# Performance work log

Measured on AMD Instinct MI355X. Metric: run time of the kernel, lower is better.

Reference implementation:

```python
import jax, jax.numpy as jnp
import numpy as np

ALPHA = 0.2  # LeakyReLU negative slope

N, Hd, Wd, T, V = 4, 16, 16, 24, 32


def setup_inputs() -> dict:
    key = jax.random.key(0)
    k1, k2, k3 = jax.random.split(key, 3)
    h = jax.random.normal(k1, (N, Hd, Wd, T, V), dtype=jnp.float32)
    W_param = jax.random.normal(k2, (T, T), dtype=jnp.float32) * 0.1
    a_param = jax.random.normal(k3, (2 * Hd * Wd, 1), dtype=jnp.float32) * 0.1
    B_param = jnp.zeros((V, V), dtype=jnp.float32)
    return {"h": h, "W_param": W_param, "a_param": a_param, "B_param": B_param}


def reference(h, W_param, a_param, B_param):
    n, H, W, T_, V_ = h.shape
    hv = jnp.transpose(h, (0, 4, 1, 2, 3))  # (N,V,H,W,T)
    Wh = hv @ W_param                        # (N,V,H,W,T), contracts last dim T

    # batch_prepare_attentional_mechanism_input (faithful to the torch view):
    rep_chunks = jnp.repeat(Wh, V_, axis=1)          # (N,V*V,H,W,T) -> i index
    rep_alt = jnp.tile(Wh, (1, V_, 1, 1, 1))          # (N,V*V,H,W,T) -> j index
    a_input = jnp.concatenate([rep_chunks, rep_alt], axis=-2)  # (N,V*V,H,2W,T)
    a_input = a_input.reshape(n, V_, V_, T_, 2 * H * W)        # raw row-major view

    e = jnp.squeeze(a_input @ a_param, -1)            # (N,V,V,T)
    e = jnp.where(e > 0, e, ALPHA * e)                # LeakyReLU
    att = jax.nn.softmax(e, axis=-1)                  # softmax over T (dim=-1)

    # adjacency: B + I, min-max normalized, symmetric D^{-1/2} A D^{-1/2}
    adj = B_param + 1e-6 + jnp.eye(V_, dtype=h.dtype)
    adj = (adj - adj.min()) / (adj.max() - adj.min())
    dinv = 1.0 / jnp.sqrt(jnp.sum(adj, axis=1))
    adj_norm = adj * dinv[:, None] * dinv[None, :]

    # nested per-node loop collapsed: matmul with diag_embed(att) == per-t scaling
    Whf = Wh.reshape(n, V_, H * W, T_)
    hp = jnp.einsum('njpt,nijt->nipt', Whf, att)      # (N,V,HW,T)
    h2 = jnp.einsum('nipt,iv->nptv', hp, adj_norm)    # (N,HW,T,V)
    h2 = h2.reshape(n, H, W, T_, V_)
    return jax.nn.sigmoid(jax.nn.elu(h2))
```

## Files before the change

kernel.cpp:

```cpp
#include <hip/hip_runtime.h>
#include <math.h>

#define ALPHA 0.2f

#define NB 4
#define TT 24
#define VV 32
#define HW 256

#define WS_WH    0
#define WS_EPART 786432
#define WS_ATT   983040
#define WS_ADJN  1081344

__global__ __launch_bounds__(256) void k1_wh_e(
    const float* __restrict__ h, const float* __restrict__ Wp,
    const float* __restrict__ ap, float* __restrict__ ws)
{
  __shared__ float WL[576];
  __shared__ float aL[512];
  __shared__ float EiL[768];
  __shared__ float EjL[768];

  const int b   = blockIdx.x;
  const int n   = b >> 5;
  const int pt  = b & 31;
  const int p0  = pt * 8;
  const int tid = threadIdx.x;
  const int v   = tid & 31;
  const int g   = tid >> 5;
  const int p   = p0 + g;

  for (int idx = tid; idx < 576; idx += 256) WL[idx] = Wp[idx];
  for (int idx = tid; idx < 512; idx += 256) aL[idx] = ap[idx];
  for (int idx = tid; idx < 768; idx += 256) { EiL[idx] = 0.f; EjL[idx] = 0.f; }

  float hrow[24];
  const float* hp = h + (size_t)(n * HW + p) * TT * VV + v;
  #pragma unroll
  for (int t2 = 0; t2 < 24; ++t2) hrow[t2] = hp[t2 * 32];

  __syncthreads();

  float acc[24];
  #pragma unroll
  for (int t = 0; t < 24; ++t) acc[t] = 0.f;
  #pragma unroll
  for (int t2 = 0; t2 < 24; ++t2) {
    const float hv = hrow[t2];
    const float4* wrow = (const float4*)&WL[t2 * 24];
    #pragma unroll
    for (int q = 0; q < 6; ++q) {
      float4 w4 = wrow[q];
      acc[q*4+0] += hv * w4.x; acc[q*4+1] += hv * w4.y;
      acc[q*4+2] += hv * w4.z; acc[q*4+3] += hv * w4.w;
    }
  }

  const int hh = p >> 4, w = p & 15;
  const int qi0 = hh * 768 + w * 24;
  const int qj0 = qi0 + 384;
  const int tti0 = qi0 >> 9;
  const int ttj0 = qj0 >> 9;
  const bool cri = (((qi0 + 23) >> 9) != tti0);
  const bool crj = (((qj0 + 23) >> 9) != ttj0);

  float ai0 = 0.f, ai1 = 0.f, aj0 = 0.f, aj1 = 0.f;

  float* whout = ws + WS_WH + (size_t)n * TT * HW * VV + (size_t)p * VV + v;
  #pragma unroll
  for (int t = 0; t < 24; ++t) {
    const float wh = acc[t];
    whout[(size_t)t * HW * VV] = wh;
    const int qi = qi0 + t;
    const float ci = aL[qi & 511] * wh;
    const bool si = ((qi >> 9) != tti0);
    ai0 += si ? 0.f : ci;  ai1 += si ? ci : 0.f;
    const int qj = qj0 + t;
    const float cj = aL[qj & 511] * wh;
    const bool sj = ((qj >> 9) != ttj0);
    aj0 += sj ? 0.f : cj;  aj1 += sj ? cj : 0.f;
  }

  atomicAdd(&EiL[v * 24 + tti0], ai0);
  if (cri) atomicAdd(&EiL[v * 24 + tti0 + 1], ai1);
  atomicAdd(&EjL[v * 24 + ttj0], aj0);
  if (crj) atomicAdd(&EjL[v * 24 + ttj0 + 1], aj1);
  __syncthreads();

  float* ep = ws + WS_EPART + (size_t)b * 1536;
  for (int idx = tid; idx < 768; idx += 256) {
    ep[idx]       = EiL[idx];
    ep[768 + idx] = EjL[idx];
  }
}

__global__ __launch_bounds__(256) void k2_att(
    const float* __restrict__ Bp, float* __restrict__ ws)
{
  __shared__ float E[2 * 32 * 25];
  __shared__ float adjw[1024];
  __shared__ float dinvL[32];
  __shared__ float redmn[4], redmx[4];
  __shared__ float smn, smx;

  const int n = blockIdx.x;
  const int tid = threadIdx.x;

  const float* ep = ws + WS_EPART + (size_t)n * 32 * 1536;
  for (int o = tid; o < 1536; o += 256) {
    float s = 0.f;
    #pragma unroll 4
    for (int k = 0; k < 32; ++k) s += ep[(size_t)k * 1536 + o];
    const int side = o >> 9 >= 1 ? (o >= 768 ? 1 : 0) : 0;
    const int rem = o - (o >= 768 ? 768 : 0);
    const int vv = rem / 24, t = rem - vv * 24;
    E[(o >= 768 ? 800 : 0) + vv * 25 + t] = s;
    (void)side;
  }

  float lmn = 1e30f, lmx = -1e30f;
  if (n == 0) {
    for (int o = tid; o < 1024; o += 256) {
      const int i = o >> 5, j = o & 31;
      const float x = Bp[o] + 1e-6f + (i == j ? 1.f : 0.f);
      adjw[o] = x;
      lmn = fminf(lmn, x); lmx = fmaxf(lmx, x);
    }
    #pragma unroll
    for (int off = 32; off > 0; off >>= 1) {
      lmn = fminf(lmn, __shfl_down(lmn, off));
      lmx = fmaxf(lmx, __shfl_down(lmx, off));
    }
    if ((tid & 63) == 0) { redmn[tid >> 6] = lmn; redmx[tid >> 6] = lmx; }
  }
  __syncthreads();
  if (n == 0 && tid == 0) {
    smn = fminf(fminf(redmn[0], redmn[1]), fminf(redmn[2], redmn[3]));
    smx = fmaxf(fmaxf(redmx[0], redmx[1]), fmaxf(redmx[2], redmx[3]));
  }
  __syncthreads();
  if (n == 0) {
    const float rs = 1.f / (smx - smn);
    for (int o = tid; o < 1024; o += 256) adjw[o] = (adjw[o] - smn) * rs;
  }
  __syncthreads();
  if (n == 0 && tid < 32) {
    float s = 0.f;
    #pragma unroll
    for (int j = 0; j < 32; ++j) s += adjw[tid * 32 + j];
    dinvL[tid] = rsqrtf(s);
  }
  __syncthreads();
  if (n == 0) {
    for (int o = tid; o < 1024; o += 256) {
      const int i = o >> 5, j = o & 31;
      ws[WS_ADJN + o] = adjw[o] * dinvL[i] * dinvL[j];
    }
  }

  for (int pair = tid; pair < 1024; pair += 256) {
    const int i = pair >> 5, j = pair & 31;
    const float* Ei = &E[i * 25];
    const float* Ej = &E[800 + j * 25];
    float ev[24];
    float mx = -1e30f;
    #pragma unroll
    for (int t = 0; t < 24; ++t) {
      float x = Ei[t] + Ej[t];
      x = x > 0.f ? x : ALPHA * x;
      ev[t] = x; mx = fmaxf(mx, x);
    }
    float s = 0.f;
    #pragma unroll
    for (int t = 0; t < 24; ++t) { const float e = __expf(ev[t] - mx); ev[t] = e; s += e; }
    const float r = 1.f / s;
    float* attout = ws + WS_ATT + (size_t)n * TT * 1024 + pair;
    #pragma unroll
    for (int t = 0; t < 24; ++t) attout[(size_t)t * 1024] = ev[t] * r;
  }
}

__global__ __launch_bounds__(256) void k3_out(
    float* __restrict__ out, const float* __restrict__ ws)
{
  __shared__ float attL[1024];
  __shared__ float adjnL[1024];
  __shared__ float MT[1024];
  __shared__ float WhL[8192];

  const int b = blockIdx.x;
  const int n = b / 24, t = b - n * 24;
  const int tid = threadIdx.x;

  const float* attg = ws + WS_ATT + (size_t)(n * 24 + t) * 1024;
  for (int o = tid; o < 1024; o += 256) {
    attL[o]  = attg[o];
    adjnL[o] = ws[WS_ADJN + o];
  }
  const float4* wh4 = (const float4*)(ws + WS_WH + (size_t)(n * 24 + t) * 8192);
  float4* whl4 = (float4*)WhL;
  for (int o = tid; o < 2048; o += 256) whl4[o] = wh4[o];
  __syncthreads();

  for (int o = tid; o < 1024; o += 256) {
    const int j = o >> 5, v = o & 31;
    float s = 0.f;
    #pragma unroll
    for (int i = 0; i < 32; ++i) s += adjnL[i * 32 + v] * attL[i * 32 + j];
    MT[o] = s;
  }
  __syncthreads();

  const int v = tid & 31, g = tid >> 5;
  float mv[32];
  #pragma unroll
  for (int jj = 0; jj < 32; ++jj) mv[jj] = MT[jj * 32 + v];

  float* outg = out + (size_t)n * HW * TT * VV + (size_t)t * VV + v;
  #pragma unroll 4
  for (int k = 0; k < 32; ++k) {
    const int p = (g << 5) + k;
    const float4* wr = (const float4*)&WhL[p * 32];
    float accv = 0.f;
    #pragma unroll
    for (int q = 0; q < 8; ++q) {
      float4 w4 = wr[q];
      accv += w4.x * mv[q*4+0] + w4.y * mv[q*4+1] + w4.z * mv[q*4+2] + w4.w * mv[q*4+3];
    }
    const float e  = accv > 0.f ? accv : (__expf(accv) - 1.f);
    const float sg = 1.f / (1.f + __expf(-e));
    outg[(size_t)p * TT * VV] = sg;
  }
}

extern "C" void kernel_launch(void* const* d_in, const int* in_sizes, int n_in,
                              void* d_out, int out_size, void* d_ws, size_t ws_size,
                              hipStream_t stream) {
  const float* h  = (const float*)d_in[0];
  const float* Wp = (const float*)d_in[1];
  const float* ap = (const float*)d_in[2];
  const float* Bp = (const float*)d_in[3];
  float* out = (float*)d_out;
  float* ws  = (float*)d_ws;

  hipLaunchKernelGGL(k1_wh_e, dim3(NB * 32), dim3(256), 0, stream, h, Wp, ap, ws);
  hipLaunchKernelGGL(k2_att,  dim3(NB),      dim3(256), 0, stream, Bp, ws);
  hipLaunchKernelGGL(k3_out,  dim3(NB * 24), dim3(256), 0, stream, out, ws);
}
```

Before: 104.2 us.

## Fuse attention softmax and adjacency normalization into the output kernel

Merges the per-batch attention kernel and the output kernel into one kernel launched per (batch, t) block. Each block recomputes the E reduction, the adjacency normalization and the softmax for its single t in shared memory, so the attention and adjacency workspace round-trips and one launch go away. In exchange the E partial-sum reduction and the softmax over all 1024 pairs are repeated 24 times per batch, and the previous stage ran on only 4 blocks.

```diff
diff --git a/kernel.cpp b/kernel.cpp
--- a/kernel.cpp
+++ b/kernel.cpp
@@ -10,8 +10,6 @@
 
 #define WS_WH    0
 #define WS_EPART 786432
-#define WS_ATT   983040
-#define WS_ADJN  1081344
 
 __global__ __launch_bounds__(256) void k1_wh_e(
     const float* __restrict__ h, const float* __restrict__ Wp,
@@ -95,70 +93,75 @@
   }
 }
 
-__global__ __launch_bounds__(256) void k2_att(
-    const float* __restrict__ Bp, float* __restrict__ ws)
+__global__ __launch_bounds__(256) void k2_fused(
+    const float* __restrict__ Bp, float* __restrict__ out,
+    const float* __restrict__ ws)
 {
-  __shared__ float E[2 * 32 * 25];
+  __shared__ float E[1600];
   __shared__ float adjw[1024];
+  __shared__ float attL[1024];
+  __shared__ float MT[1024];
+  __shared__ float WhL[8192];
   __shared__ float dinvL[32];
   __shared__ float redmn[4], redmx[4];
   __shared__ float smn, smx;
 
-  const int n = blockIdx.x;
+  const int b = blockIdx.x;
+  const int n = b / 24, t = b - n * 24;
   const int tid = threadIdx.x;
+
+  const float4* wh4 = (const float4*)(ws + WS_WH + (size_t)(n * 24 + t) * 8192);
+  float4* whl4 = (float4*)WhL;
+  for (int o = tid; o < 2048; o += 256) whl4[o] = wh4[o];
 
   const float* ep = ws + WS_EPART + (size_t)n * 32 * 1536;
   for (int o = tid; o < 1536; o += 256) {
     float s = 0.f;
-    #pragma unroll 4
+    #pragma unroll 8
     for (int k = 0; k < 32; ++k) s += ep[(size_t)k * 1536 + o];
-    const int side = o >> 9 >= 1 ? (o >= 768 ? 1 : 0) : 0;
-    const int rem = o - (o >= 768 ? 768 : 0);
-    const int vv = rem / 24, t = rem - vv * 24;
-    E[(o >= 768 ? 800 : 0) + vv * 25 + t] = s;
-    (void)side;
+    const int side = (o >= 768) ? 1 : 0;
+    const int rem = o - side * 768;
+    const int vv = rem / 24, tt = rem - vv * 24;
+    E[side * 800 + vv * 25 + tt] = s;
   }
 
   float lmn = 1e30f, lmx = -1e30f;
-  if (n == 0) {
-    for (int o = tid; o < 1024; o += 256) {
-      const int i = o >> 5, j = o & 31;
-      const float x = Bp[o] + 1e-6f + (i == j ? 1.f : 0.f);
-      adjw[o] = x;
-      lmn = fminf(lmn, x); lmx = fmaxf(lmx, x);
-    }
-    #pragma unroll
-    for (int off = 32; off > 0; off >>= 1) {
-      lmn = fminf(lmn, __shfl_down(lmn, off));
-      lmx = fmaxf(lmx, __shfl_down(lmx, off));
-    }
-    if ((tid & 63) == 0) { redmn[tid >> 6] = lmn; redmx[tid >> 6] = lmx; }
-  }
-  __syncthreads();
-  if (n == 0 && tid == 0) {
+  for (int o = tid; o < 1024; o += 256) {
+    const int i = o >> 5, j = o & 31;
+    const float x = Bp[o] + 1e-6f + (i == j ? 1.f : 0.f);
+    adjw[o] = x;
+    lmn = fminf(lmn, x); lmx = fmaxf(lmx, x);
+  }
+  #pragma unroll
+  for (int off = 32; off > 0; off >>= 1) {
+    lmn = fminf(lmn, __shfl_down(lmn, off));
+    lmx = fmaxf(lmx, __shfl_down(lmx, off));
+  }
+  if ((tid & 63) == 0) { redmn[tid >> 6] = lmn; redmx[tid >> 6] = lmx; }
+  __syncthreads();
+
+  if (tid == 0) {
     smn = fminf(fminf(redmn[0], redmn[1]), fminf(redmn[2], redmn[3]));
     smx = fmaxf(fmaxf(redmx[0], redmx[1]), fmaxf(redmx[2], redmx[3]));
   }
   __syncthreads();
-  if (n == 0) {
-    const float rs = 1.f / (smx - smn);
-    for (int o = tid; o < 1024; o += 256) adjw[o] = (adjw[o] - smn) * rs;
-  }
-  __syncthreads();
-  if (n == 0 && tid < 32) {
+
+  const float rs = 1.f / (smx - smn);
+  for (int o = tid; o < 1024; o += 256) adjw[o] = (adjw[o] - smn) * rs;
+  __syncthreads();
+
+  if (tid < 32) {
     float s = 0.f;
     #pragma unroll
     for (int j = 0; j < 32; ++j) s += adjw[tid * 32 + j];
     dinvL[tid] = rsqrtf(s);
   }
   __syncthreads();
-  if (n == 0) {
-    for (int o = tid; o < 1024; o += 256) {
-      const int i = o >> 5, j = o & 31;
-      ws[WS_ADJN + o] = adjw[o] * dinvL[i] * dinvL[j];
-    }
-  }
-
+
+  for (int o = tid; o < 1024; o += 256) {
+    const int i = o >> 5, j = o & 31;
+    adjw[o] = adjw[o] * dinvL[i] * dinvL[j];
+  }
   for (int pair = tid; pair < 1024; pair += 256) {
     const int i = pair >> 5, j = pair & 31;
     const float* Ei = &E[i * 25];
@@ -166,48 +169,23 @@
     float ev[24];
     float mx = -1e30f;
     #pragma unroll
-    for (int t = 0; t < 24; ++t) {
-      float x = Ei[t] + Ej[t];
+    for (int t2 = 0; t2 < 24; ++t2) {
+      float x = Ei[t2] + Ej[t2];
       x = x > 0.f ? x : ALPHA * x;
-      ev[t] = x; mx = fmaxf(mx, x);
+      ev[t2] = x; mx = fmaxf(mx, x);
     }
     float s = 0.f;
     #pragma unroll
-    for (int t = 0; t < 24; ++t) { const float e = __expf(ev[t] - mx); ev[t] = e; s += e; }
-    const float r = 1.f / s;
-    float* attout = ws + WS_ATT + (size_t)n * TT * 1024 + pair;
-    #pragma unroll
-    for (int t = 0; t < 24; ++t) attout[(size_t)t * 1024] = ev[t] * r;
-  }
-}
-
-__global__ __launch_bounds__(256) void k3_out(
-    float* __restrict__ out, const float* __restrict__ ws)
-{
-  __shared__ float attL[1024];
-  __shared__ float adjnL[1024];
-  __shared__ float MT[1024];
-  __shared__ float WhL[8192];
-
-  const int b = blockIdx.x;
-  const int n = b / 24, t = b - n * 24;
-  const int tid = threadIdx.x;
-
-  const float* attg = ws + WS_ATT + (size_t)(n * 24 + t) * 1024;
-  for (int o = tid; o < 1024; o += 256) {
-    attL[o]  = attg[o];
-    adjnL[o] = ws[WS_ADJN + o];
-  }
-  const float4* wh4 = (const float4*)(ws + WS_WH + (size_t)(n * 24 + t) * 8192);
-  float4* whl4 = (float4*)WhL;
-  for (int o = tid; o < 2048; o += 256) whl4[o] = wh4[o];
+    for (int t2 = 0; t2 < 24; ++t2) { const float e = __expf(ev[t2] - mx); ev[t2] = e; s += e; }
+    attL[pair] = ev[t] / s;
+  }
   __syncthreads();
 
   for (int o = tid; o < 1024; o += 256) {
     const int j = o >> 5, v = o & 31;
     float s = 0.f;
     #pragma unroll
-    for (int i = 0; i < 32; ++i) s += adjnL[i * 32 + v] * attL[i * 32 + j];
+    for (int i = 0; i < 32; ++i) s += adjw[i * 32 + v] * attL[i * 32 + j];
     MT[o] = s;
   }
   __syncthreads();
@@ -244,7 +222,6 @@
   float* out = (float*)d_out;
   float* ws  = (float*)d_ws;
 
-  hipLaunchKernelGGL(k1_wh_e, dim3(NB * 32), dim3(256), 0, stream, h, Wp, ap, ws);
-  hipLaunchKernelGGL(k2_att,  dim3(NB),      dim3(256), 0, stream, Bp, ws);
-  hipLaunchKernelGGL(k3_out,  dim3(NB * 24), dim3(256), 0, stream, out, ws);
+  hipLaunchKernelGGL(k1_wh_e,  dim3(NB * 32), dim3(256), 0, stream, h, Wp, ap, ws);
+  hipLaunchKernelGGL(k2_fused, dim3(NB * 24), dim3(256), 0, stream, Bp, out, ws);
 }
```

Result: faster. 98.55 us (-5.4%).
